# Kernel optimization log

Measured on AMD Instinct MI355X. Metric: run time of the kernel, lower is better.

## Reference

```python
import jax, jax.numpy as jnp
import numpy as np

B, L, F, H = 8, 1024, 1024, 16
D = F // H  # head dim = 64

def setup_inputs() -> dict:
    key = jax.random.key(0)
    k1, k2, k3, k4 = jax.random.split(key, 4)
    x = jax.random.normal(k1, (B, L, F), jnp.float32)
    # lecun_normal-style scaling for projections
    w_qkv = jax.random.normal(k2, (F, 3 * F), jnp.float32) / jnp.sqrt(F)
    # relative position bias table: (2*window-1, heads)
    rpe_table = jax.random.normal(k3, (2 * L - 1, H), jnp.float32) * 0.02
    w_out = jax.random.normal(k4, (F, F), jnp.float32) / jnp.sqrt(F)
    return {"x": x, "w_qkv": w_qkv, "rpe_table": rpe_table, "w_out": w_out}

def reference(x, w_qkv, rpe_table, w_out):
    # QKV projection (use_bias=False)
    qkv = jnp.einsum('blf,fe->ble', x, w_qkv)              # [B, L, 3F]
    qkv = qkv.reshape(B, L, H, 3 * D)
    q, k, v = jnp.split(qkv, 3, axis=-1)                   # each [B, L, H, D]
    q = q / jnp.sqrt(jnp.asarray(D, x.dtype))
    # relative positional bias: gather table at index (i - j + L - 1)
    rel_idx = jnp.arange(L)[:, None] - jnp.arange(L)[None, :] + (L - 1)  # [L, L]
    bias = jnp.transpose(rpe_table[rel_idx], (2, 0, 1))    # [H, L, L]
    scores = jnp.einsum('bqhd,bkhd->bhqk', q, k) + bias[None]  # [B, H, L, L]
    attn = jax.nn.softmax(scores, axis=-1)
    out = jnp.einsum('bhqk,bkhd->bqhd', attn, v)           # [B, L, H, D]
    out = out.reshape(B, L, F)
    return jnp.einsum('blf,fo->blo', out, w_out)
```

## Files before the change

kernel.cpp:

```cpp
#include <hip/hip_runtime.h>


typedef __attribute__((ext_vector_type(8))) short bf16x8;
typedef __attribute__((ext_vector_type(4))) float f32x4;
typedef unsigned short u16;
typedef unsigned int u32;

__device__ __forceinline__ u16 f2bf(float f) {
  u32 u = __builtin_bit_cast(u32, f);
  u = (u + 0x7fffu + ((u >> 16) & 1u)) >> 16;
  return (u16)u;
}

__device__ __forceinline__ f32x4 mfma16(bf16x8 a, bf16x8 b, f32x4 c) {
  return __builtin_amdgcn_mfma_f32_16x16x32_bf16(a, b, c, 0, 0, 0);
}

__device__ __forceinline__ void gld_lds16(const u16* g, u16* l) {
  __builtin_amdgcn_global_load_lds(
      (const __attribute__((address_space(1))) unsigned int*)g,
      (__attribute__((address_space(3))) unsigned int*)l, 16, 0, 0);
}

#define BARRIER() asm volatile("s_barrier" ::: "memory")
#define VMCNT4() asm volatile("s_waitcnt vmcnt(4)" ::: "memory")
#define VMCNT0() asm volatile("s_waitcnt vmcnt(0)" ::: "memory")

__global__ __launch_bounds__(256) void cast_kernel(const float* __restrict__ in,
                                                   u16* __restrict__ out, int n8) {
  int i = blockIdx.x * 256 + threadIdx.x;
  if (i >= n8) return;
  float4 a = ((const float4*)in)[2 * i];
  float4 b = ((const float4*)in)[2 * i + 1];
  uint4 o;
  o.x = (u32)f2bf(a.x) | ((u32)f2bf(a.y) << 16);
  o.y = (u32)f2bf(a.z) | ((u32)f2bf(a.w) << 16);
  o.z = (u32)f2bf(b.x) | ((u32)f2bf(b.y) << 16);
  o.w = (u32)f2bf(b.z) | ((u32)f2bf(b.w) << 16);
  ((uint4*)out)[i] = o;
}

__global__ __launch_bounds__(256) void transpose_cast_kernel(const float* __restrict__ in,
                                                             u16* __restrict__ out,
                                                             int R, int C) {
  __shared__ float tile[32][33];
  const int c0 = blockIdx.x * 32, r0 = blockIdx.y * 32;
  const int tx = threadIdx.x, ty = threadIdx.y;
#pragma unroll
  for (int i = 0; i < 32; i += 8)
    tile[ty + i][tx] = in[(size_t)(r0 + ty + i) * C + (c0 + tx)];
  __syncthreads();
#pragma unroll
  for (int i = 0; i < 32; i += 8)
    out[(size_t)(c0 + ty + i) * R + (r0 + tx)] = f2bf(tile[tx][ty + i]);
}

__global__ __launch_bounds__(256) void rpe_prep_kernel(const float* __restrict__ rpe,
                                                       float* __restrict__ rpeT) {
  int o = blockIdx.x * 256 + threadIdx.x;
  int h = o >> 11, i = o & 2047;
  if (i < 2047) rpeT[h * 2048 + i] = rpe[(size_t)i * 16 + h] * 1.44269504f;
}

template <int EPI>
__global__ __launch_bounds__(512, 2) void gemm2_kernel(const u16* __restrict__ A,
                                                       const u16* __restrict__ BT,
                                                       void* __restrict__ C0,
                                                       void* __restrict__ C1,
                                                       int M, int N, int K, int ny) {
  __shared__ u16 LA[2][256][64];
  __shared__ u16 LB[2][256][64];
  const int tid = threadIdx.x, lane = tid & 63, w = tid >> 6;
  const int wm = w >> 2, wn = w & 3;
  const int l15 = lane & 15, l4 = lane >> 4;
  const int e7 = l15 & 7;

  const int nwg = gridDim.x;
  const int virt = ((int)blockIdx.x & 7) * (nwg >> 3) + ((int)blockIdx.x >> 3);
  const int bx = virt / ny, by = virt % ny;
  const int bm0 = by * 256, bn0 = bx * 256;
  const int nt = K >> 6;

  const int sr = tid >> 3, sc = tid & 7;

  auto stageA = [&](int buf, int half, int kt) {
#pragma unroll
    for (int s = 0; s < 2; ++s) {
      int r = s * 64 + sr;
      gld_lds16(A + (size_t)(bm0 + half * 128 + r) * K + kt * 64 + ((sc ^ (r & 7)) * 8),
                &LA[buf][half * 128][0] + s * 4096 + tid * 8);
    }
  };
  auto stageB = [&](int buf, int half, int kt) {
#pragma unroll
    for (int s = 0; s < 2; ++s) {
      int r = s * 64 + sr;
      gld_lds16(BT + (size_t)(bn0 + half * 128 + r) * K + kt * 64 + ((sc ^ (r & 7)) * 8),
                &LB[buf][half * 128][0] + s * 4096 + tid * 8);
    }
  };

  const f32x4 zero = {0.f, 0.f, 0.f, 0.f};
  f32x4 acc[8][4];
#pragma unroll
  for (int i = 0; i < 8; ++i)
#pragma unroll
    for (int j = 0; j < 4; ++j) acc[i][j] = zero;

  bf16x8 afr[8], bf0[4], bf1[4];

  auto ldA = [&](int bt, int mh) {
#pragma unroll
    for (int mi2 = 0; mi2 < 4; ++mi2)
#pragma unroll
      for (int ks = 0; ks < 2; ++ks)
        afr[mi2 * 2 + ks] = *(const bf16x8*)&LA[bt][wm * 128 + mh * 64 + mi2 * 16 + l15]
                                               [((ks * 4 + l4) ^ e7) * 8];
  };
  auto ldB = [&](int bt, int nh, bf16x8* bfr) {
#pragma unroll
    for (int ni2 = 0; ni2 < 2; ++ni2)
#pragma unroll
      for (int ks = 0; ks < 2; ++ks)
        bfr[ni2 * 2 + ks] = *(const bf16x8*)&LB[bt][wn * 64 + (nh * 2 + ni2) * 16 + l15]
                                                [((ks * 4 + l4) ^ e7) * 8];
  };
  auto quad = [&](int mh, int nh, bf16x8* bfr) {
    __builtin_amdgcn_s_setprio(1);
#pragma unroll
    for (int mi2 = 0; mi2 < 4; ++mi2)
#pragma unroll
      for (int ni2 = 0; ni2 < 2; ++ni2)
#pragma unroll
        for (int ks = 0; ks < 2; ++ks)
          acc[mh * 4 + mi2][nh * 2 + ni2] =
              mfma16(afr[mi2 * 2 + ks], bfr[ni2 * 2 + ks], acc[mh * 4 + mi2][nh * 2 + ni2]);
    __builtin_amdgcn_s_setprio(0);
  };

  stageA(0, 0, 0);
  stageA(0, 1, 0);
  stageB(0, 0, 0);
  stageB(0, 1, 0);
  if (nt > 1) {
    stageB(1, 0, 1);
    stageB(1, 1, 1);
  }
  VMCNT4();
  BARRIER();

  for (int t = 0; t < nt; ++t) {
    const int bt = t & 1;
    ldA(bt, 0);
    ldB(bt, 0, bf0);
    if (t + 1 < nt) stageA(bt ^ 1, 0, t + 1);
    BARRIER();
    quad(0, 0, bf0);
    BARRIER();
    ldB(bt, 1, bf1);
    if (t + 1 < nt) stageA(bt ^ 1, 1, t + 1);
    BARRIER();
    quad(0, 1, bf1);
    BARRIER();
    ldA(bt, 1);
    if (t + 2 < nt) stageB(bt, 0, t + 2);
    BARRIER();
    quad(1, 0, bf0);
    BARRIER();
    if (t + 2 < nt) stageB(bt, 1, t + 2);
    if (t < nt - 2) {
      VMCNT4();
    } else {
      VMCNT0();
    }
    BARRIER();
    quad(1, 1, bf1);
    BARRIER();
  }

  const int rbase = bm0 + wm * 128 + l4 * 4;
  const int cbase = bn0 + wn * 64 + l15;
  if constexpr (EPI == 1) {
    float* C = (float*)C0;
#pragma unroll
    for (int mi = 0; mi < 8; ++mi)
#pragma unroll
      for (int reg = 0; reg < 4; ++reg)
#pragma unroll
        for (int ni = 0; ni < 4; ++ni)
          C[(size_t)(rbase + mi * 16 + reg) * N + cbase + ni * 16] = acc[mi][ni][reg];
  } else {
    u16* qkb = (u16*)C0;
    u16* vT = (u16*)C1;
    const int bq = bm0 >> 10;
    u16* bbuf = &LA[0][0][0] + w * 2048;
#pragma unroll
    for (int ni = 0; ni < 4; ++ni) {
      int n16 = bn0 + wn * 64 + ni * 16;
      int h = n16 / 192, sub = n16 - h * 192;
      if (sub < 128) {
#pragma unroll
        for (int mi = 0; mi < 8; ++mi)
#pragma unroll
          for (int reg = 0; reg < 4; ++reg) {
            int row = rbase + mi * 16 + reg;
            qkb[(size_t)row * 2048 + h * 128 + sub + l15] = f2bf(acc[mi][ni][reg]);
          }
      } else {
        asm volatile("s_waitcnt lgkmcnt(0)" ::: "memory");
#pragma unroll
        for (int mi = 0; mi < 8; ++mi)
#pragma unroll
          for (int reg = 0; reg < 4; ++reg) {
            int ml = mi * 16 + l4 * 4 + reg;
            bbuf[l15 * 128 + (((ml >> 3) ^ e7) * 8) + (ml & 7)] = f2bf(acc[mi][ni][reg]);
          }
        asm volatile("s_waitcnt lgkmcnt(0)" ::: "memory");
        int dsub = sub - 128;
#pragma unroll
        for (int pass = 0; pass < 4; ++pass) {
          int nl = lane >> 2, cc = (lane & 3) + pass * 4;
          uint4 val = *(uint4*)&bbuf[nl * 128 + ((cc ^ (nl & 7)) * 8)];
          int mg = bm0 + wm * 128 + cc * 8;
          *(uint4*)&vT[(((size_t)(bq * 16 + h) * 64 + (dsub + nl)) << 10) + (mg & 1023)] =
              val;
        }
      }
    }
  }
}

__global__ __launch_bounds__(512, 4) void attn_kernel(const u16* __restrict__ qk,
                                                      const u16* __restrict__ vT,
                                                      const float* __restrict__ rpeT,
                                                      u16* __restrict__ attn_out) {
  __shared__ u16 Ks[128][64];
  __shared__ u16 Vs[64][128];
  __shared__ u16 Ps[8][16][128];
  __shared__ float rpe_s[1152];

  const int tid = threadIdx.x, lane = tid & 63, w = tid >> 6;
  const int l15 = lane & 15, l4 = lane >> 4;
  const int bid = blockIdx.x;
  const int qt = bid >> 7, bh = bid & 127;
  const int h = bh & 15, b = bh >> 4;
  const int q0 = qt * 128;

  for (int t = tid; t < 1151; t += 512)
    rpe_s[t] = rpeT[h * 2048 + q0 + t];

  const u16* qbase = qk + ((size_t)(b * 1024 + q0 + w * 16 + l15) * 2048 + h * 128);
  bf16x8 bq0 = *(const bf16x8*)(qbase + l4 * 8);
  bf16x8 bq1 = *(const bf16x8*)(qbase + 32 + l4 * 8);

  const f32x4 zero = {0.f, 0.f, 0.f, 0.f};
  float m_run = -1e30f, l_run = 0.f;
  f32x4 oacc[4];
#pragma unroll
  for (int i = 0; i < 4; ++i) oacc[i] = zero;

  const u16* kgbase = qk + ((size_t)(b * 1024) * 2048 + h * 128 + 64);
  const u16* vgbase = vT + (size_t)bh * 65536;

  for (int kt = 0; kt < 8; ++kt) {
    const int kv0 = kt * 128;
    __syncthreads();
#pragma unroll
    for (int p = 0; p < 2; ++p) {
      int e = p * 512 + tid;
      int kr = e >> 3, kc = e & 7;
      gld_lds16(kgbase + (size_t)(kv0 + kr) * 2048 + ((kc ^ (kr & 7)) * 8),
                &Ks[0][0] + (size_t)(p * 512 + w * 64) * 8);
      int vr = e >> 4, vc = e & 15;
      gld_lds16(vgbase + (size_t)vr * 1024 + kv0 + ((vc ^ (vr & 7)) * 8),
                &Vs[0][0] + (size_t)(p * 512 + w * 64) * 8);
    }
    __syncthreads();

    f32x4 s[8];
    __builtin_amdgcn_s_setprio(1);
#pragma unroll
    for (int jt = 0; jt < 8; ++jt) {
      f32x4 t = zero;
      bf16x8 ak0 = *(const bf16x8*)&Ks[jt * 16 + l15][((l4) ^ (l15 & 7)) * 8];
      bf16x8 ak1 = *(const bf16x8*)&Ks[jt * 16 + l15][((4 + l4) ^ (l15 & 7)) * 8];
      t = mfma16(ak0, bq0, t);
      t = mfma16(ak1, bq1, t);
      s[jt] = t;
    }
    __builtin_amdgcn_s_setprio(0);

    const int ibase = w * 16 + l15 + 1023 - kv0 - l4 * 4;
#pragma unroll
    for (int jt = 0; jt < 8; ++jt)
#pragma unroll
      for (int reg = 0; reg < 4; ++reg)
        s[jt][reg] = s[jt][reg] * (0.125f * 1.44269504f) + rpe_s[ibase - jt * 16 - reg];

    float rm = fmaxf(fmaxf(s[0][0], s[0][1]), fmaxf(s[0][2], s[0][3]));
#pragma unroll
    for (int jt = 1; jt < 8; ++jt)
      rm = fmaxf(rm, fmaxf(fmaxf(s[jt][0], s[jt][1]), fmaxf(s[jt][2], s[jt][3])));
    rm = fmaxf(rm, __shfl_xor(rm, 16));
    rm = fmaxf(rm, __shfl_xor(rm, 32));

    if (__any(rm > m_run)) {
      float mnew = fmaxf(m_run, rm);
      float sc = __builtin_amdgcn_exp2f(m_run - mnew);
      m_run = mnew;
      l_run *= sc;
#pragma unroll
      for (int reg = 0; reg < 4; ++reg) {
        float scr = __shfl(sc, l4 * 4 + reg);
#pragma unroll
        for (int dt = 0; dt < 4; ++dt) oacc[dt][reg] *= scr;
      }
    }

    float rsum = 0.f;
#pragma unroll
    for (int jt = 0; jt < 8; ++jt) {
      float p0 = __builtin_amdgcn_exp2f(s[jt][0] - m_run);
      float p1 = __builtin_amdgcn_exp2f(s[jt][1] - m_run);
      float p2 = __builtin_amdgcn_exp2f(s[jt][2] - m_run);
      float p3 = __builtin_amdgcn_exp2f(s[jt][3] - m_run);
      rsum += (p0 + p1) + (p2 + p3);
      u32 pk01, pk23;
      asm("v_cvt_pk_bf16_f32 %0, %1, %2" : "=v"(pk01) : "v"(p0), "v"(p1));
      asm("v_cvt_pk_bf16_f32 %0, %1, %2" : "=v"(pk23) : "v"(p2), "v"(p3));
      int chunk = (jt * 2 + (l4 >> 1)) ^ (l15 & 7);
      u32* dst = (u32*)&Ps[w][l15][chunk * 8 + (l4 & 1) * 4];
      dst[0] = pk01;
      dst[1] = pk23;
    }
    rsum += __shfl_xor(rsum, 16);
    rsum += __shfl_xor(rsum, 32);
    l_run += rsum;

    __builtin_amdgcn_s_setprio(1);
#pragma unroll
    for (int ksv = 0; ksv < 4; ++ksv) {
      bf16x8 pa = *(const bf16x8*)&Ps[w][l15][((ksv * 4 + l4) ^ (l15 & 7)) * 8];
#pragma unroll
      for (int dt = 0; dt < 4; ++dt) {
        bf16x8 vb = *(const bf16x8*)&Vs[dt * 16 + l15][((ksv * 4 + l4) ^ (l15 & 7)) * 8];
        oacc[dt] = mfma16(pa, vb, oacc[dt]);
      }
    }
    __builtin_amdgcn_s_setprio(0);
  }

  float inv = 1.f / l_run;
#pragma unroll
  for (int reg = 0; reg < 4; ++reg) {
    float invr = __shfl(inv, l4 * 4 + reg);
    int row = b * 1024 + q0 + w * 16 + l4 * 4 + reg;
#pragma unroll
    for (int dt = 0; dt < 4; ++dt)
      attn_out[(size_t)row * 1024 + h * 64 + dt * 16 + l15] = f2bf(oacc[dt][reg] * invr);
  }
}

extern "C" void kernel_launch(void* const* d_in, const int* in_sizes, int n_in,
                              void* d_out, int out_size, void* d_ws, size_t ws_size,
                              hipStream_t stream) {
  const float* x     = (const float*)d_in[0];
  const float* w_qkv = (const float*)d_in[1];
  const float* rpe   = (const float*)d_in[2];
  const float* w_out = (const float*)d_in[3];

  char* ws = (char*)d_ws;
  u16* xb    = (u16*)(ws);
  u16* attnb = (u16*)(ws);
  u16* wqkvT = (u16*)(ws + 16777216);
  u16* woutT = (u16*)(ws + 23068672);
  float* rpeT = (float*)(ws + 23068672);
  u16* qkbuf = (u16*)(ws + 25165824);
  u16* vTbuf = (u16*)(ws + 58720256);

  cast_kernel<<<4096, 256, 0, stream>>>(x, xb, 8192 * 1024 / 8);
  dim3 tb(32, 8);
  transpose_cast_kernel<<<dim3(3072 / 32, 1024 / 32), tb, 0, stream>>>(w_qkv, wqkvT, 1024, 3072);
  rpe_prep_kernel<<<128, 256, 0, stream>>>(rpe, rpeT);

  gemm2_kernel<0><<<384, 512, 0, stream>>>(xb, wqkvT, (void*)qkbuf, (void*)vTbuf,
                                           8192, 3072, 1024, 32);

  attn_kernel<<<1024, 512, 0, stream>>>(qkbuf, vTbuf, rpeT, attnb);

  transpose_cast_kernel<<<dim3(1024 / 32, 1024 / 32), tb, 0, stream>>>(w_out, woutT, 1024, 1024);

  gemm2_kernel<1><<<128, 512, 0, stream>>>(attnb, woutT, d_out, nullptr,
                                           8192, 1024, 1024, 32);
}
```

Before: 265.9 us.

## Shrink GEMM tile to 256x128 to double workgroup count and simplify pipeline

Replaces the 256x256 GEMM tile with a 256x128 tile: the B buffer is halved, per-wave accumulators drop from 8x4 to 8x2, and the four-phase inner loop becomes two phases with a single A stage and single B stage per K step. Grid sizes double (768 for QKV, 256 for output projection), which should fill the MI355X's CUs better since the old grids of 384 and 128 workgroups underfill them, especially for the output GEMM. The cost is lower arithmetic intensity per tile, with more global/LDS traffic per FLOP and fewer MFMAs per barrier to hide latency. The epilogue's V-transpose path in LDS must still fit the smaller layout.

```diff
diff --git a/kernel.cpp b/kernel.cpp
--- a/kernel.cpp
+++ b/kernel.cpp
@@ -23,7 +23,7 @@
 }
 
 #define BARRIER() asm volatile("s_barrier" ::: "memory")
-#define VMCNT4() asm volatile("s_waitcnt vmcnt(4)" ::: "memory")
+#define VMCNT2() asm volatile("s_waitcnt vmcnt(2)" ::: "memory")
 #define VMCNT0() asm volatile("s_waitcnt vmcnt(0)" ::: "memory")
 
 __global__ __launch_bounds__(256) void cast_kernel(const float* __restrict__ in,
@@ -63,13 +63,13 @@
 }
 
 template <int EPI>
-__global__ __launch_bounds__(512, 2) void gemm2_kernel(const u16* __restrict__ A,
+__global__ __launch_bounds__(512, 2) void gemm3_kernel(const u16* __restrict__ A,
                                                        const u16* __restrict__ BT,
                                                        void* __restrict__ C0,
                                                        void* __restrict__ C1,
-                                                       int M, int N, int K, int ny) {
+                                                       int M, int N, int K) {
   __shared__ u16 LA[2][256][64];
-  __shared__ u16 LB[2][256][64];
+  __shared__ u16 LB[2][128][64];
   const int tid = threadIdx.x, lane = tid & 63, w = tid >> 6;
   const int wm = w >> 2, wn = w & 3;
   const int l15 = lane & 15, l4 = lane >> 4;
@@ -77,109 +77,95 @@
 
   const int nwg = gridDim.x;
   const int virt = ((int)blockIdx.x & 7) * (nwg >> 3) + ((int)blockIdx.x >> 3);
-  const int bx = virt / ny, by = virt % ny;
-  const int bm0 = by * 256, bn0 = bx * 256;
+  const int bx = virt >> 5, by = virt & 31;
+  const int bm0 = by * 256, bn0 = bx * 128;
   const int nt = K >> 6;
 
   const int sr = tid >> 3, sc = tid & 7;
 
-  auto stageA = [&](int buf, int half, int kt) {
+  auto stageA = [&](int buf, int kt) {
+#pragma unroll
+    for (int s = 0; s < 4; ++s) {
+      int r = s * 64 + sr;
+      gld_lds16(A + (size_t)(bm0 + r) * K + kt * 64 + ((sc ^ (r & 7)) * 8),
+                &LA[buf][0][0] + s * 4096 + tid * 8);
+    }
+  };
+  auto stageB = [&](int buf, int kt) {
 #pragma unroll
     for (int s = 0; s < 2; ++s) {
       int r = s * 64 + sr;
-      gld_lds16(A + (size_t)(bm0 + half * 128 + r) * K + kt * 64 + ((sc ^ (r & 7)) * 8),
-                &LA[buf][half * 128][0] + s * 4096 + tid * 8);
-    }
-  };
-  auto stageB = [&](int buf, int half, int kt) {
-#pragma unroll
-    for (int s = 0; s < 2; ++s) {
-      int r = s * 64 + sr;
-      gld_lds16(BT + (size_t)(bn0 + half * 128 + r) * K + kt * 64 + ((sc ^ (r & 7)) * 8),
-                &LB[buf][half * 128][0] + s * 4096 + tid * 8);
+      gld_lds16(BT + (size_t)(bn0 + r) * K + kt * 64 + ((sc ^ (r & 7)) * 8),
+                &LB[buf][0][0] + s * 4096 + tid * 8);
     }
   };
 
   const f32x4 zero = {0.f, 0.f, 0.f, 0.f};
-  f32x4 acc[8][4];
+  f32x4 acc[8][2];
 #pragma unroll
   for (int i = 0; i < 8; ++i)
 #pragma unroll
-    for (int j = 0; j < 4; ++j) acc[i][j] = zero;
-
-  bf16x8 afr[8], bf0[4], bf1[4];
+    for (int j = 0; j < 2; ++j) acc[i][j] = zero;
+
+  bf16x8 afr[8], bfr[4];
 
   auto ldA = [&](int bt, int mh) {
 #pragma unroll
-    for (int mi2 = 0; mi2 < 4; ++mi2)
+    for (int mi = 0; mi < 4; ++mi)
 #pragma unroll
       for (int ks = 0; ks < 2; ++ks)
-        afr[mi2 * 2 + ks] = *(const bf16x8*)&LA[bt][wm * 128 + mh * 64 + mi2 * 16 + l15]
-                                               [((ks * 4 + l4) ^ e7) * 8];
-  };
-  auto ldB = [&](int bt, int nh, bf16x8* bfr) {
-#pragma unroll
-    for (int ni2 = 0; ni2 < 2; ++ni2)
+        afr[mi * 2 + ks] = *(const bf16x8*)&LA[bt][wm * 128 + mh * 64 + mi * 16 + l15]
+                                              [((ks * 4 + l4) ^ e7) * 8];
+  };
+  auto ldB = [&](int bt) {
+#pragma unroll
+    for (int ni = 0; ni < 2; ++ni)
 #pragma unroll
       for (int ks = 0; ks < 2; ++ks)
-        bfr[ni2 * 2 + ks] = *(const bf16x8*)&LB[bt][wn * 64 + (nh * 2 + ni2) * 16 + l15]
-                                                [((ks * 4 + l4) ^ e7) * 8];
-  };
-  auto quad = [&](int mh, int nh, bf16x8* bfr) {
+        bfr[ni * 2 + ks] = *(const bf16x8*)&LB[bt][wn * 32 + ni * 16 + l15]
+                                              [((ks * 4 + l4) ^ e7) * 8];
+  };
+  auto quad = [&](int mh) {
     __builtin_amdgcn_s_setprio(1);
 #pragma unroll
-    for (int mi2 = 0; mi2 < 4; ++mi2)
-#pragma unroll
-      for (int ni2 = 0; ni2 < 2; ++ni2)
+    for (int mi = 0; mi < 4; ++mi)
+#pragma unroll
+      for (int ni = 0; ni < 2; ++ni)
 #pragma unroll
         for (int ks = 0; ks < 2; ++ks)
-          acc[mh * 4 + mi2][nh * 2 + ni2] =
-              mfma16(afr[mi2 * 2 + ks], bfr[ni2 * 2 + ks], acc[mh * 4 + mi2][nh * 2 + ni2]);
+          acc[mh * 4 + mi][ni] =
+              mfma16(afr[mi * 2 + ks], bfr[ni * 2 + ks], acc[mh * 4 + mi][ni]);
     __builtin_amdgcn_s_setprio(0);
   };
 
-  stageA(0, 0, 0);
-  stageA(0, 1, 0);
-  stageB(0, 0, 0);
-  stageB(0, 1, 0);
-  if (nt > 1) {
-    stageB(1, 0, 1);
-    stageB(1, 1, 1);
-  }
-  VMCNT4();
+  stageA(0, 0);
+  stageB(0, 0);
+  if (nt > 1) stageB(1, 1);
+  VMCNT2();
   BARRIER();
 
   for (int t = 0; t < nt; ++t) {
     const int bt = t & 1;
     ldA(bt, 0);
-    ldB(bt, 0, bf0);
-    if (t + 1 < nt) stageA(bt ^ 1, 0, t + 1);
+    ldB(bt);
+    if (t + 1 < nt) stageA(bt ^ 1, t + 1);
     BARRIER();
-    quad(0, 0, bf0);
-    BARRIER();
-    ldB(bt, 1, bf1);
-    if (t + 1 < nt) stageA(bt ^ 1, 1, t + 1);
-    BARRIER();
-    quad(0, 1, bf1);
+    quad(0);
     BARRIER();
     ldA(bt, 1);
-    if (t + 2 < nt) stageB(bt, 0, t + 2);
-    BARRIER();
-    quad(1, 0, bf0);
-    BARRIER();
-    if (t + 2 < nt) stageB(bt, 1, t + 2);
-    if (t < nt - 2) {
-      VMCNT4();
+    if (t + 2 < nt) {
+      stageB(bt, t + 2);
+      VMCNT2();
     } else {
       VMCNT0();
     }
     BARRIER();
-    quad(1, 1, bf1);
+    quad(1);
     BARRIER();
   }
 
   const int rbase = bm0 + wm * 128 + l4 * 4;
-  const int cbase = bn0 + wn * 64 + l15;
+  const int cbase = bn0 + wn * 32 + l15;
   if constexpr (EPI == 1) {
     float* C = (float*)C0;
 #pragma unroll
@@ -187,7 +173,7 @@
 #pragma unroll
       for (int reg = 0; reg < 4; ++reg)
 #pragma unroll
-        for (int ni = 0; ni < 4; ++ni)
+        for (int ni = 0; ni < 2; ++ni)
           C[(size_t)(rbase + mi * 16 + reg) * N + cbase + ni * 16] = acc[mi][ni][reg];
   } else {
     u16* qkb = (u16*)C0;
@@ -195,8 +181,8 @@
     const int bq = bm0 >> 10;
     u16* bbuf = &LA[0][0][0] + w * 2048;
 #pragma unroll
-    for (int ni = 0; ni < 4; ++ni) {
-      int n16 = bn0 + wn * 64 + ni * 16;
+    for (int ni = 0; ni < 2; ++ni) {
+      int n16 = bn0 + wn * 32 + ni * 16;
       int h = n16 / 192, sub = n16 - h * 192;
       if (sub < 128) {
 #pragma unroll
@@ -383,13 +369,13 @@
   transpose_cast_kernel<<<dim3(3072 / 32, 1024 / 32), tb, 0, stream>>>(w_qkv, wqkvT, 1024, 3072);
   rpe_prep_kernel<<<128, 256, 0, stream>>>(rpe, rpeT);
 
-  gemm2_kernel<0><<<384, 512, 0, stream>>>(xb, wqkvT, (void*)qkbuf, (void*)vTbuf,
-                                           8192, 3072, 1024, 32);
+  gemm3_kernel<0><<<768, 512, 0, stream>>>(xb, wqkvT, (void*)qkbuf, (void*)vTbuf,
+                                           8192, 3072, 1024);
 
   attn_kernel<<<1024, 512, 0, stream>>>(qkbuf, vTbuf, rpeT, attnb);
 
   transpose_cast_kernel<<<dim3(1024 / 32, 1024 / 32), tb, 0, stream>>>(w_out, woutT, 1024, 1024);
 
-  gemm2_kernel<1><<<128, 512, 0, stream>>>(attnb, woutT, d_out, nullptr,
-                                           8192, 1024, 1024, 32);
-}
+  gemm3_kernel<1><<<256, 512, 0, stream>>>(attnb, woutT, d_out, nullptr,
+                                           8192, 1024, 1024);
+}
```

After: 263.0 us. No clear change (-1.1%).
